# Performance work log

Measured on AMD Instinct MI355X. Metric: run time of the kernel, lower is better.

Reference implementation:

```python
import jax, jax.numpy as jnp
import numpy as np

H = 1024
V = 50000
E_SOUND, E_NUM = 40, 5
D_SOUND, D_NUM = 32, 32
IN_DIM = H + D_SOUND + D_NUM  # GRU input size
B, L = 128, 128


def setup_inputs() -> dict:
    key = jax.random.key(0)
    ks = jax.random.split(key, 16)
    s = lambda k, shape: jax.random.normal(k, shape, jnp.float32) * 0.02
    return {
        "input_seq": jax.random.randint(ks[0], (B,), 0, V),
        "last_hidden": jax.random.normal(ks[1], (1, B, H), jnp.float32),
        "encoder_outputs": jax.random.normal(ks[2], (L, B, H), jnp.float32),
        "char2num": jax.random.randint(ks[3], (V,), 0, E_NUM),
        "char2final": jax.random.randint(ks[4], (V,), 0, E_SOUND),
        "emb": s(ks[5], (V, H)),
        "sound_emb": s(ks[6], (E_SOUND, D_SOUND)),
        "num_emb": s(ks[7], (E_NUM, D_NUM)),
        "W_ih": s(ks[8], (3 * H, IN_DIM)),
        "W_hh": s(ks[9], (3 * H, H)),
        "b_ih": jnp.zeros((3 * H,), jnp.float32),
        "b_hh": jnp.zeros((3 * H,), jnp.float32),
        "W_attn": s(ks[10], (H, H)),
        "b_attn": jnp.zeros((H,), jnp.float32),
        "W_cat": s(ks[11], (H, 2 * H)),
        "b_cat": jnp.zeros((H,), jnp.float32),
        "W_out": s(ks[12], (V, H)),
        "b_out": jnp.zeros((V,), jnp.float32),
    }


def _gru_cell(x, h, W_ih, W_hh, b_ih, b_hh):
    # PyTorch GRU gate order: r, z, n
    gi = x @ W_ih.T + b_ih
    gh = h @ W_hh.T + b_hh
    i_r, i_z, i_n = jnp.split(gi, 3, axis=-1)
    h_r, h_z, h_n = jnp.split(gh, 3, axis=-1)
    r = jax.nn.sigmoid(i_r + h_r)
    z = jax.nn.sigmoid(i_z + h_z)
    n = jnp.tanh(i_n + r * h_n)
    return (1.0 - z) * n + z * h


def reference(input_seq, last_hidden, encoder_outputs, char2num, char2final,
              emb, sound_emb, num_emb, W_ih, W_hh, b_ih, b_hh,
              W_attn, b_attn, W_cat, b_cat, W_out, b_out):
    # Embeddings (eval mode -> dropout is identity)
    e = emb[input_seq]                             # [B,H]
    num_ids = char2num[input_seq]                  # [B]
    snd_ids = char2final[input_seq]                # [B]
    x = jnp.concatenate([e, sound_emb[snd_ids], num_emb[num_ids]], -1)  # [B,IN_DIM]

    # Single-step single-layer GRU
    h_new = _gru_cell(x, last_hidden[0], W_ih, W_hh, b_ih, b_hh)  # [B,H]
    hidden = h_new[None]                            # [1,B,H]
    rnn_output = h_new                              # [B,H]

    # Luong 'general' attention, batched (replaces the nested-loop .mm calls)
    proj = jnp.einsum('lbh,kh->lbk', encoder_outputs, W_attn) + b_attn  # [L,B,H]
    energies = jnp.einsum('bh,lbh->bl', rnn_output, proj)               # [B,L]
    attn_weights = jax.nn.softmax(energies, axis=1)[:, None, :]         # [B,1,L]
    context = jnp.einsum('bl,lbh->bh', attn_weights[:, 0], encoder_outputs)

    concat_out = jnp.tanh(jnp.concatenate([rnn_output, context], -1) @ W_cat.T + b_cat)
    output = concat_out @ W_out.T + b_out           # [B,V]
    return output, hidden, attn_weights
```

## Files before the change

### kernel.cpp

```cpp
#include <hip/hip_runtime.h>
#include <hip/hip_bf16.h>
#include <cstddef>

#define B_   128
#define L_   128
#define H_   1024
#define V_   50000
#define INDIM 1088

typedef short short8 __attribute__((ext_vector_type(8)));
typedef unsigned short ushort8 __attribute__((ext_vector_type(8)));
typedef unsigned short ushort4v __attribute__((ext_vector_type(4)));
typedef float f32x4 __attribute__((ext_vector_type(4)));

static __device__ __forceinline__ unsigned short f2bf(float f) {
    unsigned u = __builtin_bit_cast(unsigned, f);
    u = u + 0x7FFFu + ((u >> 16) & 1u);
    return (unsigned short)(u >> 16);
}
static __device__ __forceinline__ float bf2f(unsigned short h) {
    unsigned u = ((unsigned)h) << 16;
    return __builtin_bit_cast(float, u);
}
static __device__ __forceinline__ float sigm(float v) {
    return 1.f / (1.f + __expf(-v));
}

__global__ __launch_bounds__(256) void prep_kernel(
    const int* __restrict__ seq, const int* __restrict__ c2n,
    const int* __restrict__ c2f, const float* __restrict__ emb,
    const float* __restrict__ semb, const float* __restrict__ nemb,
    const float* __restrict__ lh,
    unsigned short* __restrict__ x_hi, unsigned short* __restrict__ x_lo,
    unsigned short* __restrict__ h_hi, unsigned short* __restrict__ h_lo)
{
    const int b = blockIdx.x, t = threadIdx.x;
    const int idx = seq[b];
    for (int i = t; i < 528; i += 256) {
        float4 v;
        unsigned short *dh, *dl;
        int off;
        if (i < 272) {
            if (i < 256) {
                v = *(const float4*)&emb[(size_t)idx * H_ + i * 4];
            } else {
                const int j = i - 256;
                if (j < 8) v = *(const float4*)&semb[c2f[idx] * 32 + j * 4];
                else       v = *(const float4*)&nemb[c2n[idx] * 32 + (j - 8) * 4];
            }
            dh = x_hi + (size_t)b * INDIM; dl = x_lo + (size_t)b * INDIM; off = i * 4;
        } else {
            const int j = i - 272;
            v = *(const float4*)&lh[(size_t)b * H_ + j * 4];
            dh = h_hi + (size_t)b * H_; dl = h_lo + (size_t)b * H_; off = j * 4;
        }
        const float fv[4] = {v.x, v.y, v.z, v.w};
        ushort4v hh, ll;
#pragma unroll
        for (int e = 0; e < 4; e++) {
            hh[e] = f2bf(fv[e]);
            ll[e] = f2bf(fv[e] - bf2f(hh[e]));
        }
        *(ushort4v*)&dh[off] = hh;
        *(ushort4v*)&dl[off] = ll;
    }
}

template<bool WT, bool SPLIT, bool TANH>
__global__ __launch_bounds__(256, SPLIT ? 2 : 4) void sgemm(
    const unsigned short* __restrict__ Ah, const unsigned short* __restrict__ Al, int lda,
    const float* __restrict__ W, int ldw,
    const float* __restrict__ bias,
    float* __restrict__ C, int ldc, size_t pstride,
    int N, int k_len0, int k_lenB)
{
    __shared__ unsigned short As_h[128][72];
    __shared__ unsigned short Ws_h[64][72];
    __shared__ unsigned short As_l[SPLIT ? 128 : 1][72];
    __shared__ unsigned short Ws_l[SPLIT ? 64 : 1][72];

    const int t    = threadIdx.x;
    const int lane = t & 63;
    const int wv   = t >> 6;
    const int wr   = wv >> 1;
    const int wc   = wv & 1;
    const int n0   = blockIdx.x * 64;
    const int l15  = lane & 15;
    const int g    = lane >> 4;

    const int y     = blockIdx.y;
    const int k_off = (y == 0) ? 0 : k_len0 + (y - 1) * k_lenB;
    const int k_len = (y == 0) ? k_len0 : k_lenB;
    float* Cp = C + (size_t)y * pstride;

    const int ar = t >> 3;
    const int ac = (t & 7) * 8;
    const int wn = t >> 2, wq = t & 3;
    const int nk = t >> 4, nn4 = (t & 15) * 4;

    f32x4 acc[4][2];
#pragma unroll
    for (int i = 0; i < 4; i++)
#pragma unroll
        for (int j = 0; j < 2; j++) acc[i][j] = (f32x4){0.f, 0.f, 0.f, 0.f};

#define LOAD_REGS(K0, RA, RAL, RW) do {                                        \
    _Pragma("unroll")                                                          \
    for (int i_ = 0; i_ < 4; i_++)                                             \
        RA[i_] = *(const ushort8*)&Ah[(size_t)(ar + i_ * 32) * lda + (K0) + ac]; \
    if constexpr (SPLIT) {                                                     \
        _Pragma("unroll")                                                      \
        for (int i_ = 0; i_ < 4; i_++)                                         \
            RAL[i_] = *(const ushort8*)&Al[(size_t)(ar + i_ * 32) * lda + (K0) + ac]; \
    }                                                                          \
    if constexpr (WT) {                                                        \
        const bool ok_ = (n0 + wn) < N;                                        \
        const float* wb_ = W + (size_t)(n0 + wn) * ldw + (K0);                 \
        _Pragma("unroll")                                                      \
        for (int j_ = 0; j_ < 4; j_++)                                         \
            RW[j_] = ok_ ? *(const float4*)&wb_[j_ * 16 + wq * 4]              \
                         : make_float4(0.f, 0.f, 0.f, 0.f);                    \
    } else {                                                                   \
        _Pragma("unroll")                                                      \
        for (int j_ = 0; j_ < 4; j_++)                                         \
            RW[j_] = *(const float4*)&W[(size_t)((K0) + nk + j_ * 16) * ldw + n0 + nn4]; \
    }                                                                          \
} while (0)

#define STAGE_REGS(RA, RAL, RW) do {                                           \
    _Pragma("unroll")                                                          \
    for (int i_ = 0; i_ < 4; i_++) {                                           \
        *(ushort8*)&As_h[ar + i_ * 32][ac] = RA[i_];                           \
        if constexpr (SPLIT) *(ushort8*)&As_l[ar + i_ * 32][ac] = RAL[i_];     \
    }                                                                          \
    if constexpr (WT) {                                                        \
        _Pragma("unroll")                                                      \
        for (int j_ = 0; j_ < 4; j_++) {                                       \
            const float fv_[4] = {RW[j_].x, RW[j_].y, RW[j_].z, RW[j_].w};     \
            ushort4v hh_, ll_;                                                 \
            _Pragma("unroll")                                                  \
            for (int e_ = 0; e_ < 4; e_++) {                                   \
                hh_[e_] = f2bf(fv_[e_]);                                       \
                if constexpr (SPLIT) ll_[e_] = f2bf(fv_[e_] - bf2f(hh_[e_]));  \
            }                                                                  \
            *(ushort4v*)&Ws_h[wn][j_ * 16 + wq * 4] = hh_;                     \
            if constexpr (SPLIT) *(ushort4v*)&Ws_l[wn][j_ * 16 + wq * 4] = ll_; \
        }                                                                      \
    } else {                                                                   \
        _Pragma("unroll")                                                      \
        for (int j_ = 0; j_ < 4; j_++) {                                       \
            const float fv_[4] = {RW[j_].x, RW[j_].y, RW[j_].z, RW[j_].w};     \
            _Pragma("unroll")                                                  \
            for (int e_ = 0; e_ < 4; e_++) {                                   \
                const unsigned short hb_ = f2bf(fv_[e_]);                      \
                Ws_h[nn4 + e_][nk + j_ * 16] = hb_;                            \
                if constexpr (SPLIT)                                           \
                    Ws_l[nn4 + e_][nk + j_ * 16] = f2bf(fv_[e_] - bf2f(hb_));  \
            }                                                                  \
        }                                                                      \
    }                                                                          \
} while (0)

    ushort8 ra[4], ral[4];
    float4 rw[4];
    LOAD_REGS(k_off, ra, ral, rw);

    const int k_end = k_off + k_len;
    for (int k0 = k_off; k0 < k_end; k0 += 64) {
        ushort8 nb[4], nbl[4];
        float4 nw[4];
        const bool more = (k0 + 64) < k_end;
        if (more) LOAD_REGS(k0 + 64, nb, nbl, nw);

        STAGE_REGS(ra, ral, rw);
        __syncthreads();

#pragma unroll
        for (int ks = 0; ks < 2; ks++) {
            const int ko = ks * 32 + g * 8;
            short8 ah[4], bh[2];
#pragma unroll
            for (int mi = 0; mi < 4; mi++)
                ah[mi] = *(const short8*)&As_h[wr * 64 + mi * 16 + l15][ko];
#pragma unroll
            for (int ni = 0; ni < 2; ni++)
                bh[ni] = *(const short8*)&Ws_h[wc * 32 + ni * 16 + l15][ko];
            if constexpr (SPLIT) {
                short8 al[4], bl[2];
#pragma unroll
                for (int mi = 0; mi < 4; mi++)
                    al[mi] = *(const short8*)&As_l[wr * 64 + mi * 16 + l15][ko];
#pragma unroll
                for (int ni = 0; ni < 2; ni++)
                    bl[ni] = *(const short8*)&Ws_l[wc * 32 + ni * 16 + l15][ko];
#pragma unroll
                for (int mi = 0; mi < 4; mi++)
#pragma unroll
                    for (int ni = 0; ni < 2; ni++) {
                        acc[mi][ni] = __builtin_amdgcn_mfma_f32_16x16x32_bf16(ah[mi], bh[ni], acc[mi][ni], 0, 0, 0);
                        acc[mi][ni] = __builtin_amdgcn_mfma_f32_16x16x32_bf16(ah[mi], bl[ni], acc[mi][ni], 0, 0, 0);
                        acc[mi][ni] = __builtin_amdgcn_mfma_f32_16x16x32_bf16(al[mi], bh[ni], acc[mi][ni], 0, 0, 0);
                    }
            } else {
#pragma unroll
                for (int mi = 0; mi < 4; mi++)
#pragma unroll
                    for (int ni = 0; ni < 2; ni++)
                        acc[mi][ni] = __builtin_amdgcn_mfma_f32_16x16x32_bf16(ah[mi], bh[ni], acc[mi][ni], 0, 0, 0);
            }
        }
        __syncthreads();

        if (more) {
#pragma unroll
            for (int i = 0; i < 4; i++) {
                ra[i] = nb[i];
                if constexpr (SPLIT) ral[i] = nbl[i];
            }
#pragma unroll
            for (int j = 0; j < 4; j++) rw[j] = nw[j];
        }
    }
#undef LOAD_REGS
#undef STAGE_REGS

#pragma unroll
    for (int mi = 0; mi < 4; mi++) {
#pragma unroll
        for (int ni = 0; ni < 2; ni++) {
            const int col = n0 + wc * 32 + ni * 16 + l15;
            if (col < N) {
                const float bb = bias ? bias[col] : 0.f;
#pragma unroll
                for (int r = 0; r < 4; r++) {
                    const int row = wr * 64 + mi * 16 + g * 4 + r;
                    float v = acc[mi][ni][r] + bb;
                    if (TANH) v = tanhf(v);
                    Cp[(size_t)row * ldc + col] = v;
                }
            }
        }
    }
}

__global__ __launch_bounds__(256) void gru_gates_kernel(
    const float* __restrict__ gi, const float* __restrict__ gh,
    const float* __restrict__ b_ih, const float* __restrict__ b_hh,
    const float* __restrict__ h_prev,
    float* __restrict__ hid_out,
    unsigned short* __restrict__ cat_hi, unsigned short* __restrict__ cat_lo)
{
    const int id = blockIdx.x * 256 + threadIdx.x;
    const int b = id >> 10, j = id & 1023;
    const size_t base = (size_t)b * 3072 + j;
    float ir = b_ih[j], iz = b_ih[1024 + j], in_ = b_ih[2048 + j];
    float hr = b_hh[j], hz = b_hh[1024 + j], hn = b_hh[2048 + j];
#pragma unroll
    for (int p = 0; p < 4; p++) {
        const float* gp = gi + (size_t)p * (128 * 3072);
        const float* hp = gh + (size_t)p * (128 * 3072);
        ir += gp[base]; iz += gp[base + 1024]; in_ += gp[base + 2048];
        hr += hp[base]; hz += hp[base + 1024]; hn += hp[base + 2048];
    }
    const float r = sigm(ir + hr);
    const float z = sigm(iz + hz);
    const float n = tanhf(in_ + r * hn);
    const float h = (1.f - z) * n + z * h_prev[id];
    hid_out[id] = h;
    const unsigned short hb = f2bf(h);
    cat_hi[(size_t)b * 2048 + j] = hb;
    cat_lo[(size_t)b * 2048 + j] = f2bf(h - bf2f(hb));
}

__global__ __launch_bounds__(256) void energy_partial_kernel(
    const float* __restrict__ qp, const float* __restrict__ enc,
    float* __restrict__ epart)
{
    const int s = blockIdx.x, b = blockIdx.y;
    const int t = threadIdx.x, lane = t & 63, wv = t >> 6;
    __shared__ float q_s[256];
    {
        const size_t o = (size_t)b * H_ + s * 256 + t;
        q_s[t] = qp[o] + qp[o + 131072] + qp[o + 262144] + qp[o + 393216];
    }
    __syncthreads();
    const float4 qv = *(const float4*)&q_s[lane * 4];
    const float* encb = enc + (size_t)b * H_ + s * 256;
    for (int l0 = 0; l0 < 32; l0++) {
        const int l = wv * 32 + l0;
        float4 ev = *(const float4*)&encb[(size_t)l * (B_ * H_) + lane * 4];
        float p = ev.x * qv.x + ev.y * qv.y + ev.z * qv.z + ev.w * qv.w;
#pragma unroll
        for (int off = 32; off > 0; off >>= 1) p += __shfl_xor(p, off);
        if (lane == 0) epart[((size_t)b * 128 + l) * 4 + s] = p;
    }
}

__global__ __launch_bounds__(128) void attn_softmax_kernel(
    const float* __restrict__ epart, float* __restrict__ attnw)
{
    const int b = blockIdx.x, t = threadIdx.x;
    const int lane = t & 63, wv = t >> 6;
    __shared__ float red[2];
    float4 pe = *(const float4*)&epart[((size_t)b * 128 + t) * 4];
    const float e = pe.x + pe.y + pe.z + pe.w;
    float mx = e;
#pragma unroll
    for (int off = 32; off > 0; off >>= 1) mx = fmaxf(mx, __shfl_xor(mx, off));
    if (lane == 0) red[wv] = mx;
    __syncthreads();
    const float gm = fmaxf(red[0], red[1]);
    __syncthreads();
    const float ex = __expf(e - gm);
    float sm = ex;
#pragma unroll
    for (int off = 32; off > 0; off >>= 1) sm += __shfl_xor(sm, off);
    if (lane == 0) red[wv] = sm;
    __syncthreads();
    attnw[(size_t)b * L_ + t] = ex / (red[0] + red[1]);
}

__global__ __launch_bounds__(256) void context_kernel(
    const float* __restrict__ attnw, const float* __restrict__ enc,
    unsigned short* __restrict__ cat_hi)
{
    const int s = blockIdx.x, b = blockIdx.y, t = threadIdx.x;
    __shared__ float w_s[128];
    if (t < 128) w_s[t] = attnw[(size_t)b * L_ + t];
    __syncthreads();
    const int h = s * 256 + t;
    const float* encb = enc + (size_t)b * H_ + h;
    float c = 0.f;
#pragma unroll 4
    for (int l = 0; l < 128; l++)
        c += w_s[l] * encb[(size_t)l * (B_ * H_)];
    cat_hi[(size_t)b * 2048 + 1024 + h] = f2bf(c);
}

__global__ __launch_bounds__(256) void co_reduce_kernel(
    const float* __restrict__ co_part, const float* __restrict__ b_cat,
    unsigned short* __restrict__ co_hi)
{
    const int id = blockIdx.x * 256 + threadIdx.x;
    const int j = id & 1023;
    float s = b_cat[j];
#pragma unroll
    for (int p = 0; p < 4; p++) s += co_part[(size_t)p * 131072 + id];
    co_hi[id] = f2bf(tanhf(s));
}

extern "C" void kernel_launch(void* const* d_in, const int* in_sizes, int n_in,
                              void* d_out, int out_size, void* d_ws, size_t ws_size,
                              hipStream_t stream)
{
    const int*   seq    = (const int*)  d_in[0];
    const float* lh     = (const float*)d_in[1];
    const float* enc    = (const float*)d_in[2];
    const int*   c2n    = (const int*)  d_in[3];
    const int*   c2f    = (const int*)  d_in[4];
    const float* emb    = (const float*)d_in[5];
    const float* semb   = (const float*)d_in[6];
    const float* nemb   = (const float*)d_in[7];
    const float* W_ih   = (const float*)d_in[8];
    const float* W_hh   = (const float*)d_in[9];
    const float* b_ih   = (const float*)d_in[10];
    const float* b_hh   = (const float*)d_in[11];
    const float* W_attn = (const float*)d_in[12];
    const float* W_cat  = (const float*)d_in[14];
    const float* b_cat  = (const float*)d_in[15];
    const float* W_out  = (const float*)d_in[16];
    const float* b_out  = (const float*)d_in[17];

    float* out    = (float*)d_out;
    float* hidden = out + (size_t)B_ * V_;
    float* attnw  = hidden + (size_t)B_ * H_;

    unsigned short* x_hi   = (unsigned short*)d_ws;
    unsigned short* x_lo   = x_hi   + (size_t)128 * INDIM;
    unsigned short* h_hi   = x_lo   + (size_t)128 * INDIM;
    unsigned short* h_lo   = h_hi   + (size_t)128 * 1024;
    unsigned short* cat_hi = h_lo   + (size_t)128 * 1024;
    unsigned short* cat_lo = cat_hi + (size_t)128 * 2048;
    unsigned short* co_hi  = cat_lo + (size_t)128 * 2048;
    float* fbase   = (float*)(co_hi + (size_t)128 * 1024);
    float* gi_part = fbase;
    float* gh_part = gi_part + (size_t)4 * 128 * 3072;
    float* q_part  = fbase;
    float* co_part = q_part + (size_t)4 * 128 * 1024;
    float* epart   = co_part + (size_t)4 * 128 * 1024;

    hipLaunchKernelGGL(prep_kernel, dim3(B_), dim3(256), 0, stream,
                       seq, c2n, c2f, emb, semb, nemb, lh, x_hi, x_lo, h_hi, h_lo);
    hipLaunchKernelGGL((sgemm<true, true, false>), dim3(48, 4), dim3(256), 0, stream,
                       x_hi, x_lo, INDIM, W_ih, INDIM, (const float*)nullptr,
                       gi_part, 3072, (size_t)128 * 3072, 3072, 320, 256);
    hipLaunchKernelGGL((sgemm<true, true, false>), dim3(48, 4), dim3(256), 0, stream,
                       h_hi, h_lo, H_, W_hh, H_, (const float*)nullptr,
                       gh_part, 3072, (size_t)128 * 3072, 3072, 256, 256);
    hipLaunchKernelGGL(gru_gates_kernel, dim3(512), dim3(256), 0, stream,
                       gi_part, gh_part, b_ih, b_hh, lh, hidden, cat_hi, cat_lo);
    hipLaunchKernelGGL((sgemm<false, true, false>), dim3(16, 4), dim3(256), 0, stream,
                       cat_hi, cat_lo, 2048, W_attn, H_, (const float*)nullptr,
                       q_part, H_, (size_t)128 * 1024, H_, 256, 256);
    hipLaunchKernelGGL(energy_partial_kernel, dim3(4, 128), dim3(256), 0, stream,
                       q_part, enc, epart);
    hipLaunchKernelGGL(attn_softmax_kernel, dim3(128), dim3(128), 0, stream,
                       epart, attnw);
    hipLaunchKernelGGL(context_kernel, dim3(4, 128), dim3(256), 0, stream,
                       attnw, enc, cat_hi);
    hipLaunchKernelGGL((sgemm<true, false, false>), dim3(16, 4), dim3(256), 0, stream,
                       cat_hi, cat_hi, 2048, W_cat, 2048, (const float*)nullptr,
                       co_part, H_, (size_t)128 * 1024, H_, 512, 512);
    hipLaunchKernelGGL(co_reduce_kernel, dim3(512), dim3(256), 0, stream,
                       co_part, b_cat, co_hi);
    hipLaunchKernelGGL((sgemm<true, false, false>), dim3((V_ + 63) / 64, 1), dim3(256), 0, stream,
                       co_hi, co_hi, H_, W_out, H_, b_out,
                       out, V_, (size_t)0, V_, H_, H_);
}
```

Measured before the change: 175.2 us.

## Merge GRU GEMMs, deepen weight prefetch, fuse softmax into context kernel

Merges the two GRU input and hidden GEMMs into one launch, selected by blockIdx.z. Adds a two-stage-deep register prefetch of fp32 weights for the non-split GEMM, which includes the large W_out projection. Moves shared memory to dynamic allocation so the plain GEMM requests less LDS. Also fuses the softmax into the context kernel, doubles the threads in the energy kernel, and changes launch bounds for the non-split GEMM from 4 to 2 waves per SIMD. The extra prefetch registers and the lower occupancy hint could hurt latency hiding.

```diff
diff --git a/kernel.cpp b/kernel.cpp
--- a/kernel.cpp
+++ b/kernel.cpp
@@ -67,17 +67,19 @@
 }
 
 template<bool WT, bool SPLIT, bool TANH>
-__global__ __launch_bounds__(256, SPLIT ? 2 : 4) void sgemm(
+static __device__ __forceinline__ void sgemm_body(
     const unsigned short* __restrict__ Ah, const unsigned short* __restrict__ Al, int lda,
     const float* __restrict__ W, int ldw,
     const float* __restrict__ bias,
     float* __restrict__ C, int ldc, size_t pstride,
     int N, int k_len0, int k_lenB)
 {
-    __shared__ unsigned short As_h[128][72];
-    __shared__ unsigned short Ws_h[64][72];
-    __shared__ unsigned short As_l[SPLIT ? 128 : 1][72];
-    __shared__ unsigned short Ws_l[SPLIT ? 64 : 1][72];
+    extern __shared__ char smem_raw[];
+    typedef unsigned short RowT[72];
+    RowT* As_h = (RowT*)(smem_raw);
+    RowT* Ws_h = (RowT*)(smem_raw + 18432);
+    RowT* As_l = (RowT*)(smem_raw + 27648);
+    RowT* Ws_l = (RowT*)(smem_raw + 46080);
 
     const int t    = threadIdx.x;
     const int lane = t & 63;
@@ -104,7 +106,7 @@
 #pragma unroll
         for (int j = 0; j < 2; j++) acc[i][j] = (f32x4){0.f, 0.f, 0.f, 0.f};
 
-#define LOAD_REGS(K0, RA, RAL, RW) do {                                        \
+#define LOAD_A(K0, RA, RAL) do {                                               \
     _Pragma("unroll")                                                          \
     for (int i_ = 0; i_ < 4; i_++)                                             \
         RA[i_] = *(const ushort8*)&Ah[(size_t)(ar + i_ * 32) * lda + (K0) + ac]; \
@@ -113,6 +115,9 @@
         for (int i_ = 0; i_ < 4; i_++)                                         \
             RAL[i_] = *(const ushort8*)&Al[(size_t)(ar + i_ * 32) * lda + (K0) + ac]; \
     }                                                                          \
+} while (0)
+
+#define LOAD_W(K0, RW) do {                                                    \
     if constexpr (WT) {                                                        \
         const bool ok_ = (n0 + wn) < N;                                        \
         const float* wb_ = W + (size_t)(n0 + wn) * ldw + (K0);                 \
@@ -161,19 +166,31 @@
     }                                                                          \
 } while (0)
 
-    ushort8 ra[4], ral[4];
-    float4 rw[4];
-    LOAD_REGS(k_off, ra, ral, rw);
-
     const int k_end = k_off + k_len;
+
+    ushort8 ra[4], ral[4], nra[4], nral[4];
+    float4 rw0[4], rw1[4], rw2[4];
+
+    LOAD_A(k_off, ra, ral);
+    LOAD_W(k_off, rw0);
+    if constexpr (!SPLIT) {
+        if (k_off + 64 < k_end) LOAD_W(k_off + 64, rw1);
+    }
+
     for (int k0 = k_off; k0 < k_end; k0 += 64) {
-        ushort8 nb[4], nbl[4];
-        float4 nw[4];
-        const bool more = (k0 + 64) < k_end;
-        if (more) LOAD_REGS(k0 + 64, nb, nbl, nw);
-
-        STAGE_REGS(ra, ral, rw);
+        const bool m1 = (k0 + 64) < k_end;
+        const bool m2 = (k0 + 128) < k_end;
+        if (m1) {
+            LOAD_A(k0 + 64, nra, nral);
+            if constexpr (SPLIT) LOAD_W(k0 + 64, rw1);
+        }
+
+        STAGE_REGS(ra, ral, rw0);
         __syncthreads();
+
+        if constexpr (!SPLIT) {
+            if (m2) LOAD_W(k0 + 128, rw2);
+        }
 
 #pragma unroll
         for (int ks = 0; ks < 2; ks++) {
@@ -211,17 +228,21 @@
         }
         __syncthreads();
 
-        if (more) {
+        if (m1) {
 #pragma unroll
             for (int i = 0; i < 4; i++) {
-                ra[i] = nb[i];
-                if constexpr (SPLIT) ral[i] = nbl[i];
+                ra[i] = nra[i];
+                if constexpr (SPLIT) ral[i] = nral[i];
             }
 #pragma unroll
-            for (int j = 0; j < 4; j++) rw[j] = nw[j];
-        }
-    }
-#undef LOAD_REGS
+            for (int j = 0; j < 4; j++) {
+                rw0[j] = rw1[j];
+                if constexpr (!SPLIT) rw1[j] = rw2[j];
+            }
+        }
+    }
+#undef LOAD_A
+#undef LOAD_W
 #undef STAGE_REGS
 
 #pragma unroll
@@ -241,6 +262,32 @@
             }
         }
     }
+}
+
+template<bool WT, bool SPLIT, bool TANH>
+__global__ __launch_bounds__(256, 2) void sgemm(
+    const unsigned short* __restrict__ Ah, const unsigned short* __restrict__ Al, int lda,
+    const float* __restrict__ W, int ldw,
+    const float* __restrict__ bias,
+    float* __restrict__ C, int ldc, size_t pstride,
+    int N, int k_len0, int k_lenB)
+{
+    sgemm_body<WT, SPLIT, TANH>(Ah, Al, lda, W, ldw, bias, C, ldc, pstride, N, k_len0, k_lenB);
+}
+
+__global__ __launch_bounds__(256, 2) void gru_gemm(
+    const unsigned short* __restrict__ x_hi, const unsigned short* __restrict__ x_lo,
+    const float* __restrict__ W_ih,
+    const unsigned short* __restrict__ h_hi, const unsigned short* __restrict__ h_lo,
+    const float* __restrict__ W_hh,
+    float* __restrict__ gi, float* __restrict__ gh)
+{
+    if (blockIdx.z == 0)
+        sgemm_body<true, true, false>(x_hi, x_lo, INDIM, W_ih, INDIM, nullptr,
+                                      gi, 3072, (size_t)128 * 3072, 3072, 320, 256);
+    else
+        sgemm_body<true, true, false>(h_hi, h_lo, H_, W_hh, H_, nullptr,
+                                      gh, 3072, (size_t)128 * 3072, 3072, 256, 256);
 }
 
 __global__ __launch_bounds__(256) void gru_gates_kernel(
@@ -272,22 +319,22 @@
     cat_lo[(size_t)b * 2048 + j] = f2bf(h - bf2f(hb));
 }
 
-__global__ __launch_bounds__(256) void energy_partial_kernel(
+__global__ __launch_bounds__(512) void energy_partial_kernel(
     const float* __restrict__ qp, const float* __restrict__ enc,
     float* __restrict__ epart)
 {
     const int s = blockIdx.x, b = blockIdx.y;
     const int t = threadIdx.x, lane = t & 63, wv = t >> 6;
     __shared__ float q_s[256];
-    {
+    if (t < 256) {
         const size_t o = (size_t)b * H_ + s * 256 + t;
         q_s[t] = qp[o] + qp[o + 131072] + qp[o + 262144] + qp[o + 393216];
     }
     __syncthreads();
     const float4 qv = *(const float4*)&q_s[lane * 4];
     const float* encb = enc + (size_t)b * H_ + s * 256;
-    for (int l0 = 0; l0 < 32; l0++) {
-        const int l = wv * 32 + l0;
+    for (int l0 = 0; l0 < 16; l0++) {
+        const int l = wv * 16 + l0;
         float4 ev = *(const float4*)&encb[(size_t)l * (B_ * H_) + lane * 4];
         float p = ev.x * qv.x + ev.y * qv.y + ev.z * qv.z + ev.w * qv.w;
 #pragma unroll
@@ -296,38 +343,41 @@
     }
 }
 
-__global__ __launch_bounds__(128) void attn_softmax_kernel(
-    const float* __restrict__ epart, float* __restrict__ attnw)
-{
-    const int b = blockIdx.x, t = threadIdx.x;
+__global__ __launch_bounds__(256) void context_softmax_kernel(
+    const float* __restrict__ epart, const float* __restrict__ enc,
+    unsigned short* __restrict__ cat_hi, float* __restrict__ attnw)
+{
+    const int s = blockIdx.x, b = blockIdx.y, t = threadIdx.x;
     const int lane = t & 63, wv = t >> 6;
-    __shared__ float red[2];
-    float4 pe = *(const float4*)&epart[((size_t)b * 128 + t) * 4];
-    const float e = pe.x + pe.y + pe.z + pe.w;
+    __shared__ float w_s[128];
+    __shared__ float red[4];
+
+    float e = -INFINITY;
+    if (t < 128) {
+        float4 pe = *(const float4*)&epart[((size_t)b * 128 + t) * 4];
+        e = pe.x + pe.y + pe.z + pe.w;
+    }
     float mx = e;
 #pragma unroll
     for (int off = 32; off > 0; off >>= 1) mx = fmaxf(mx, __shfl_xor(mx, off));
     if (lane == 0) red[wv] = mx;
     __syncthreads();
-    const float gm = fmaxf(red[0], red[1]);
+    const float gm = fmaxf(fmaxf(red[0], red[1]), fmaxf(red[2], red[3]));
     __syncthreads();
-    const float ex = __expf(e - gm);
+    float ex = (t < 128) ? __expf(e - gm) : 0.f;
     float sm = ex;
 #pragma unroll
     for (int off = 32; off > 0; off >>= 1) sm += __shfl_xor(sm, off);
     if (lane == 0) red[wv] = sm;
     __syncthreads();
-    attnw[(size_t)b * L_ + t] = ex / (red[0] + red[1]);
-}
-
-__global__ __launch_bounds__(256) void context_kernel(
-    const float* __restrict__ attnw, const float* __restrict__ enc,
-    unsigned short* __restrict__ cat_hi)
-{
-    const int s = blockIdx.x, b = blockIdx.y, t = threadIdx.x;
-    __shared__ float w_s[128];
-    if (t < 128) w_s[t] = attnw[(size_t)b * L_ + t];
+    const float gs = red[0] + red[1] + red[2] + red[3];
+    if (t < 128) {
+        const float w = ex / gs;
+        w_s[t] = w;
+        if (s == 0) attnw[(size_t)b * L_ + t] = w;
+    }
     __syncthreads();
+
     const int h = s * 256 + t;
     const float* encb = enc + (size_t)b * H_ + h;
     float c = 0.f;
@@ -389,31 +439,28 @@
     float* co_part = q_part + (size_t)4 * 128 * 1024;
     float* epart   = co_part + (size_t)4 * 128 * 1024;
 
+    const int SMEM_SPLIT = 55296;
+    const int SMEM_PLAIN = 27648;
+
     hipLaunchKernelGGL(prep_kernel, dim3(B_), dim3(256), 0, stream,
                        seq, c2n, c2f, emb, semb, nemb, lh, x_hi, x_lo, h_hi, h_lo);
-    hipLaunchKernelGGL((sgemm<true, true, false>), dim3(48, 4), dim3(256), 0, stream,
-                       x_hi, x_lo, INDIM, W_ih, INDIM, (const float*)nullptr,
-                       gi_part, 3072, (size_t)128 * 3072, 3072, 320, 256);
-    hipLaunchKernelGGL((sgemm<true, true, false>), dim3(48, 4), dim3(256), 0, stream,
-                       h_hi, h_lo, H_, W_hh, H_, (const float*)nullptr,
-                       gh_part, 3072, (size_t)128 * 3072, 3072, 256, 256);
+    hipLaunchKernelGGL(gru_gemm, dim3(48, 4, 2), dim3(256), SMEM_SPLIT, stream,
+                       x_hi, x_lo, W_ih, h_hi, h_lo, W_hh, gi_part, gh_part);
     hipLaunchKernelGGL(gru_gates_kernel, dim3(512), dim3(256), 0, stream,
                        gi_part, gh_part, b_ih, b_hh, lh, hidden, cat_hi, cat_lo);
-    hipLaunchKernelGGL((sgemm<false, true, false>), dim3(16, 4), dim3(256), 0, stream,
+    hipLaunchKernelGGL((sgemm<false, true, false>), dim3(16, 4), dim3(256), SMEM_SPLIT, stream,
                        cat_hi, cat_lo, 2048, W_attn, H_, (const float*)nullptr,
                        q_part, H_, (size_t)128 * 1024, H_, 256, 256);
-    hipLaunchKernelGGL(energy_partial_kernel, dim3(4, 128), dim3(256), 0, stream,
+    hipLaunchKernelGGL(energy_partial_kernel, dim3(4, 128), dim3(512), 0, stream,
                        q_part, enc, epart);
-    hipLaunchKernelGGL(attn_softmax_kernel, dim3(128), dim3(128), 0, stream,
-                       epart, attnw);
-    hipLaunchKernelGGL(context_kernel, dim3(4, 128), dim3(256), 0, stream,
-                       attnw, enc, cat_hi);
-    hipLaunchKernelGGL((sgemm<true, false, false>), dim3(16, 4), dim3(256), 0, stream,
+    hipLaunchKernelGGL(context_softmax_kernel, dim3(4, 128), dim3(256), 0, stream,
+                       epart, enc, cat_hi, attnw);
+    hipLaunchKernelGGL((sgemm<true, false, false>), dim3(16, 4), dim3(256), SMEM_PLAIN, stream,
                        cat_hi, cat_hi, 2048, W_cat, 2048, (const float*)nullptr,
                        co_part, H_, (size_t)128 * 1024, H_, 512, 512);
     hipLaunchKernelGGL(co_reduce_kernel, dim3(512), dim3(256), 0, stream,
                        co_part, b_cat, co_hi);
-    hipLaunchKernelGGL((sgemm<true, false, false>), dim3((V_ + 63) / 64, 1), dim3(256), 0, stream,
+    hipLaunchKernelGGL((sgemm<true, false, false>), dim3((V_ + 63) / 64, 1), dim3(256), SMEM_PLAIN, stream,
                        co_hi, co_hi, H_, W_out, H_, b_out,
                        out, V_, (size_t)0, V_, H_, H_);
 }
```

Result: faster. 160.3 us (-8.5%).
